# Optimization experiments

Measured on AMD Instinct MI355X. Metric: run time of the kernel, lower is better.

The kernel has to match this reference:

```python
import jax, jax.numpy as jnp
import numpy as np

B, S, H = 1, 1024, 2048          # batch, seq, hidden_size
I = 7168                          # intermediate_size
E = 8                             # num_local_experts
TOP_K = 2                         # num_experts_per_tok
R = int(I * H * 0.1 / (I + H))    # delta_low_rank = 159
SCALE = 0.02


def setup_inputs() -> dict:
    key = jax.random.key(0)
    ks = jax.random.split(key, 12)
    f = jnp.float32
    return {
        "x": jax.random.normal(ks[0], (B, S, H), dtype=f),
        "gate_w": jax.random.normal(ks[1], (E, H), dtype=f) * SCALE,
        "Wm1": jax.random.normal(ks[2], (I, H), dtype=f) * SCALE,  # Wmean1 (gate proj)
        "Wm2": jax.random.normal(ks[3], (H, I), dtype=f) * SCALE,  # Wmean2 (down proj)
        "Wm3": jax.random.normal(ks[4], (I, H), dtype=f) * SCALE,  # Wmean3 (up proj)
        "du1": jax.random.normal(ks[5], (E, I, R), dtype=f) * SCALE,
        "dv1": jax.random.normal(ks[6], (E, R, H), dtype=f) * SCALE,
        "du2": jax.random.normal(ks[7], (E, H, R), dtype=f) * SCALE,
        "dv2": jax.random.normal(ks[8], (E, R, I), dtype=f) * SCALE,
        "du3": jax.random.normal(ks[9], (E, I, R), dtype=f) * SCALE,
        "dv3": jax.random.normal(ks[10], (E, R, H), dtype=f) * SCALE,
    }


def reference(x, gate_w, Wm1, Wm2, Wm3, du1, dv1, du2, dv2, du3, dv3):
    b, s, h = x.shape
    hs = x.reshape(-1, h)                                  # [T, H]

    # --- router ---
    router_logits = hs @ gate_w.T                          # [T, E]
    probs = jax.nn.softmax(router_logits.astype(jnp.float32), axis=-1)
    top_w, top_i = jax.lax.top_k(probs, TOP_K)             # [T, K]
    top_w = top_w / jnp.sum(top_w, axis=-1, keepdims=True)
    # dense combine weights [T, E]: weight of expert e for token t (0 if not selected)
    comb = jnp.sum(jax.nn.one_hot(top_i, E, dtype=top_w.dtype) * top_w[..., None], axis=1)
    comb = comb.astype(hs.dtype)

    # --- shared mean weights (computed once per token) ---
    base_gate = hs @ Wm1.T                                 # [T, I]
    base_up = hs @ Wm3.T                                   # [T, I]

    # --- per-expert low-rank deltas ---
    t1 = jnp.einsum('th,erh->ter', hs, dv1)                # [T, E, R]
    gate = base_gate[:, None, :] + jnp.einsum('ter,eir->tei', t1, du1)  # [T, E, I]
    t3 = jnp.einsum('th,erh->ter', hs, dv3)
    up = base_up[:, None, :] + jnp.einsum('ter,eir->tei', t3, du3)      # [T, E, I]

    hmid = jax.nn.silu(gate) * up                          # [T, E, I]

    out = jnp.einsum('tei,hi->teh', hmid, Wm2)             # shared down proj
    t2 = jnp.einsum('tei,eri->ter', hmid, dv2)
    out = out + jnp.einsum('ter,ehr->teh', t2, du2)        # [T, E, H]

    final = jnp.einsum('te,teh->th', comb, out).reshape(b, s, h)
    return final, router_logits
```

## Files before the change

### kernel.cpp

```cpp
#include <hip/hip_runtime.h>

#define T_TOK 1024
#define H_DIM 2048
#define I_DIM 7168
#define E_NUM 8
#define R_RANK 159
#define RP 160
#define P_PAIRS 2048

typedef __attribute__((ext_vector_type(8))) short short8;
typedef __attribute__((ext_vector_type(4))) float f32x4;

__device__ __forceinline__ ushort f2b(float f) {
  uint u = __float_as_uint(f);
  uint r = (u + 0x7FFFu + ((u >> 16) & 1u)) >> 16;
  return (ushort)r;
}
__device__ __forceinline__ float b2f(ushort u) {
  return __uint_as_float(((uint)u) << 16);
}
__device__ __forceinline__ short8 pack8(float4 a, float4 b) {
  short8 o;
  o[0] = (short)f2b(a.x); o[1] = (short)f2b(a.y); o[2] = (short)f2b(a.z); o[3] = (short)f2b(a.w);
  o[4] = (short)f2b(b.x); o[5] = (short)f2b(b.y); o[6] = (short)f2b(b.z); o[7] = (short)f2b(b.w);
  return o;
}
__device__ __forceinline__ short8 zero8() {
  short8 z;
#pragma unroll
  for (int q = 0; q < 8; ++q) z[q] = 0;
  return z;
}

#define GLOAD(gptr, lptr) \
  __builtin_amdgcn_global_load_lds((const __attribute__((address_space(1))) void*)(gptr), \
                                   (__attribute__((address_space(3))) void*)(lptr), 16, 0, 0)

__global__ __launch_bounds__(256) void router_kernel(
    const float* __restrict__ x, const float* __restrict__ gw,
    float* __restrict__ logits, float* __restrict__ comb,
    int* __restrict__ sel_e, int* __restrict__ cnt) {
  int wave = threadIdx.x >> 6, lane = threadIdx.x & 63;
  int t = blockIdx.x * 4 + wave;
  const float* xr = x + (long)t * H_DIM;
  float acc[8] = {0.f,0.f,0.f,0.f,0.f,0.f,0.f,0.f};
  for (int h = lane * 4; h < H_DIM; h += 256) {
    const float4 xv = *(const float4*)&xr[h];
#pragma unroll
    for (int e = 0; e < 8; ++e) {
      const float4 gv = *(const float4*)&gw[e * H_DIM + h];
      acc[e] += xv.x * gv.x + xv.y * gv.y + xv.z * gv.z + xv.w * gv.w;
    }
  }
#pragma unroll
  for (int off = 32; off > 0; off >>= 1)
#pragma unroll
    for (int e = 0; e < 8; ++e) acc[e] += __shfl_down(acc[e], off);
  if (lane == 0) {
#pragma unroll
    for (int e = 0; e < 8; ++e) logits[(long)t * 8 + e] = acc[e];
    int i0 = 0;
    for (int e = 1; e < 8; ++e) if (acc[e] > acc[i0]) i0 = e;
    int i1 = (i0 == 0) ? 1 : 0;
    for (int e = 0; e < 8; ++e) if (e != i0 && acc[e] > acc[i1]) i1 = e;
    float ee = __expf(acc[i1] - acc[i0]);
    float w0 = 1.f / (1.f + ee), w1 = ee / (1.f + ee);
    for (int e = 0; e < 8; ++e) comb[t * 8 + e] = 0.f;
    comb[t * 8 + i0] = w0;
    comb[t * 8 + i1] = w1;
    sel_e[t * 2] = i0;
    sel_e[t * 2 + 1] = i1;
    atomicAdd(&cnt[i0], 1);
    atomicAdd(&cnt[i1], 1);
  }
}

__global__ void init_kernel(int* cnt, int* cursor) {
  int i = threadIdx.x;
  if (i < 8) { cnt[i] = 0; cursor[i] = 0; }
}

__global__ void scan_kernel(const int* cnt, int* seg) {
  if (threadIdx.x == 0) {
    int s = 0;
    for (int e = 0; e < 8; ++e) { seg[e] = s; s += cnt[e]; }
    seg[8] = s;
  }
}

__global__ void assign_kernel(const int* __restrict__ sel_e, const float* __restrict__ comb,
                              const int* __restrict__ seg, int* __restrict__ cursor,
                              int* __restrict__ tok, float* __restrict__ wrow,
                              int* __restrict__ row_of) {
  int t = blockIdx.x * blockDim.x + threadIdx.x;
  if (t >= T_TOK) return;
  for (int k = 0; k < 2; ++k) {
    int e = sel_e[t * 2 + k];
    int pos = atomicAdd(&cursor[e], 1);
    int row = seg[e] + pos;
    tok[row] = t;
    wrow[row] = comb[t * 8 + e];
    row_of[t * 2 + k] = row;
  }
}

__global__ void cast8_kernel(const float* __restrict__ src, ushort* __restrict__ dst, long n8) {
  long idx = (long)blockIdx.x * blockDim.x + threadIdx.x;
  long stride = (long)gridDim.x * blockDim.x;
  for (long i = idx; i < n8; i += stride) {
    const float4 a = *(const float4*)&src[i * 8];
    const float4 b = *(const float4*)&src[i * 8 + 4];
    *(short8*)&dst[i * 8] = pack8(a, b);
  }
}

__global__ void padcast8_kernel(const float* __restrict__ src, ushort* __restrict__ dst, long rows) {
  long n8 = rows * (RP / 8);
  long idx = (long)blockIdx.x * blockDim.x + threadIdx.x;
  long stride = (long)gridDim.x * blockDim.x;
  for (long i = idx; i < n8; i += stride) {
    long row = i / (RP / 8);
    int c0 = (int)(i % (RP / 8)) * 8;
    short8 o;
#pragma unroll
    for (int j = 0; j < 8; ++j) {
      int c = c0 + j;
      o[j] = (c < R_RANK) ? (short)f2b(src[row * R_RANK + c]) : (short)0;
    }
    *(short8*)&dst[row * RP + c0] = o;
  }
}

__global__ void hcomb_kernel(const ushort* __restrict__ hmid, const int* __restrict__ row_of,
                             ushort* __restrict__ hc) {
  long idx = (long)blockIdx.x * blockDim.x + threadIdx.x;
  long total = (long)T_TOK * I_DIM / 8;
  if (idx >= total) return;
  long i = idx * 8;
  int t = (int)(i / I_DIM);
  int col = (int)(i % I_DIM);
  int r0 = row_of[t * 2], r1 = row_of[t * 2 + 1];
  const short8 a = *(const short8*)&hmid[(long)r0 * I_DIM + col];
  const short8 b = *(const short8*)&hmid[(long)r1 * I_DIM + col];
  short8 o;
#pragma unroll
  for (int j = 0; j < 8; ++j)
    o[j] = (short)f2b(b2f((ushort)a[j]) + b2f((ushort)b[j]));
  *(short8*)&hc[i] = o;
}

__global__ void finalfix_kernel(float* __restrict__ out, const ushort* __restrict__ delta,
                                const int* __restrict__ row_of) {
  long idx = (long)blockIdx.x * blockDim.x + threadIdx.x;
  long total = (long)T_TOK * H_DIM / 4;
  if (idx >= total) return;
  long i = idx * 4;
  int t = (int)(i / H_DIM);
  int col = (int)(i % H_DIM);
  int r0 = row_of[t * 2], r1 = row_of[t * 2 + 1];
  float4 d = *(float4*)&out[i];
  d.x += b2f(delta[(long)r0 * H_DIM + col + 0]) + b2f(delta[(long)r1 * H_DIM + col + 0]);
  d.y += b2f(delta[(long)r0 * H_DIM + col + 1]) + b2f(delta[(long)r1 * H_DIM + col + 1]);
  d.z += b2f(delta[(long)r0 * H_DIM + col + 2]) + b2f(delta[(long)r1 * H_DIM + col + 2]);
  d.w += b2f(delta[(long)r0 * H_DIM + col + 3]) + b2f(delta[(long)r1 * H_DIM + col + 3]);
  *(float4*)&out[i] = d;
}

__global__ void finalfixA_kernel(float* __restrict__ out, const float* __restrict__ dp,
                                 const ushort* __restrict__ delta, const int* __restrict__ row_of) {
  long idx = (long)blockIdx.x * blockDim.x + threadIdx.x;
  long total = (long)T_TOK * H_DIM / 4;
  if (idx >= total) return;
  long i = idx * 4;
  int t = (int)(i / H_DIM);
  int col = (int)(i % H_DIM);
  int r0 = row_of[t * 2], r1 = row_of[t * 2 + 1];
  const long plane = (long)T_TOK * H_DIM;
  float4 s = *(const float4*)&dp[i];
#pragma unroll
  for (int k = 1; k < 4; ++k) {
    const float4 q = *(const float4*)&dp[k * plane + i];
    s.x += q.x; s.y += q.y; s.z += q.z; s.w += q.w;
  }
  s.x += b2f(delta[(long)r0 * H_DIM + col + 0]) + b2f(delta[(long)r1 * H_DIM + col + 0]);
  s.y += b2f(delta[(long)r0 * H_DIM + col + 1]) + b2f(delta[(long)r1 * H_DIM + col + 1]);
  s.z += b2f(delta[(long)r0 * H_DIM + col + 2]) + b2f(delta[(long)r1 * H_DIM + col + 2]);
  s.w += b2f(delta[(long)r0 * H_DIM + col + 3]) + b2f(delta[(long)r1 * H_DIM + col + 3]);
  *(float4*)&out[i] = s;
}

template <int KS>
__global__ void reduce_cast_kernel(const float* __restrict__ P, long plane,
                                   ushort* __restrict__ out, long n) {
  long i = (long)blockIdx.x * blockDim.x + threadIdx.x;
  if (i >= n) return;
  float s = 0.f;
#pragma unroll
  for (int k = 0; k < KS; ++k) s += P[(long)k * plane + i];
  out[i] = f2b(s);
}

__global__ void reduce2_kernel(const float* __restrict__ p1, const float* __restrict__ p3,
                               ushort* __restrict__ t1g, ushort* __restrict__ t3g, long n) {
  long i = (long)blockIdx.x * blockDim.x + threadIdx.x;
  if (i >= 2 * n) return;
  const float* P = (i < n) ? p1 : p3;
  ushort* o = (i < n) ? t1g : t3g;
  long ii = (i < n) ? i : i - n;
  float s = 0.f;
#pragma unroll
  for (int k = 0; k < 8; ++k) s += P[(long)k * n + ii];
  o[ii] = f2b(s);
}


__device__ __forceinline__ void kloop_bf16(
    const ushort* ar0, const ushort* ar1,
    const ushort* br0, const ushort* br1,
    int K, ushort* As, ushort* Bs,
    int tid, int lane, int wm, int wn, f32x4 acc[4][4]) {
  for (int k0 = 0; k0 < K; k0 += 32) {
    __syncthreads();
    GLOAD(ar0 + k0, &As[tid * 8]);
    GLOAD(ar1 + k0, &As[(256 + tid) * 8]);
    GLOAD(br0 + k0, &Bs[tid * 8]);
    GLOAD(br1 + k0, &Bs[(256 + tid) * 8]);
    __syncthreads();
    short8 av[4], bv[4];
#pragma unroll
    for (int mi = 0; mi < 4; ++mi)
      av[mi] = *(const short8*)&As[(wm + mi * 16 + (lane & 15)) * 32 + (lane >> 4) * 8];
#pragma unroll
    for (int ni = 0; ni < 4; ++ni)
      bv[ni] = *(const short8*)&Bs[(wn + ni * 16 + (lane & 15)) * 32 + (lane >> 4) * 8];
#pragma unroll
    for (int mi = 0; mi < 4; ++mi)
#pragma unroll
      for (int ni = 0; ni < 4; ++ni)
        acc[mi][ni] = __builtin_amdgcn_mfma_f32_16x16x32_bf16(av[mi], bv[ni], acc[mi][ni], 0, 0, 0);
  }
}

__device__ __forceinline__ void epi_bf16(
    f32x4 acc[4][4], ushort* smem, int tid, int lane, int wm, int wn,
    int row0, int col0, int M, int Nvalid, int Npad, ushort* Cb, int ldc) {
  const int er = (lane >> 4) * 4, ec = lane & 15;
  __syncthreads();
#pragma unroll
  for (int mi = 0; mi < 4; ++mi)
#pragma unroll
    for (int ni = 0; ni < 4; ++ni)
#pragma unroll
      for (int j = 0; j < 4; ++j) {
        int rr = wm + mi * 16 + er + j;
        int c = wn + ni * 16 + ec;
        smem[rr * 128 + (c ^ ((rr & 7) << 3))] =
            (col0 + c < Nvalid) ? f2b(acc[mi][ni][j]) : (ushort)0;
      }
  __syncthreads();
  const int rl = tid >> 1, clb = (tid & 1) * 64;
  const int r = row0 + rl;
  if (r < M) {
    const int k8 = (rl & 7) << 3;
#pragma unroll
    for (int jj = 0; jj < 8; ++jj) {
      int cg = col0 + clb + jj * 8;
      if (cg < Npad) {
        short8 v = *(const short8*)&smem[rl * 128 + ((clb + jj * 8) ^ k8)];
        *(short8*)&Cb[(long)r * ldc + cg] = v;
      }
    }
  }
}


__global__ __launch_bounds__(256) void k_base(
    const ushort* __restrict__ xb, const ushort* __restrict__ w1b, const ushort* __restrict__ w3b,
    ushort* __restrict__ bgate, ushort* __restrict__ bup) {
  __shared__ ushort smem[16384];
  ushort* As = smem;
  ushort* Bs = smem + 4096;
  const ushort* B = blockIdx.z ? w3b : w1b;
  ushort* C = blockIdx.z ? bup : bgate;
  const int tid = threadIdx.x;
  const int lane = tid & 63, wave = tid >> 6;
  const int wm = (wave >> 1) * 64, wn = (wave & 1) * 64;
  const int row0 = blockIdx.y * 128, col0 = blockIdx.x * 128;
  const int sub_r = tid >> 2, sub_c = (tid & 3) * 8;
  const ushort* ar0 = xb + (long)(row0 + sub_r) * H_DIM + sub_c;
  const ushort* ar1 = xb + (long)(row0 + 64 + sub_r) * H_DIM + sub_c;
  const ushort* br0 = B + (long)(col0 + sub_r) * H_DIM + sub_c;
  const ushort* br1 = B + (long)(col0 + 64 + sub_r) * H_DIM + sub_c;
  f32x4 acc[4][4] = {};
  kloop_bf16(ar0, ar1, br0, br1, H_DIM, As, Bs, tid, lane, wm, wn, acc);
  epi_bf16(acc, smem, tid, lane, wm, wn, row0, col0, T_TOK, I_DIM, I_DIM, C, I_DIM);
}

__global__ __launch_bounds__(256) void k_t13(
    const ushort* __restrict__ xb, const ushort* __restrict__ dv1b, const ushort* __restrict__ dv3b,
    const int* __restrict__ tok, const int* __restrict__ seg, const int* __restrict__ cnt,
    float* __restrict__ p1, float* __restrict__ p3) {
  __shared__ ushort smem[8192];
  ushort* As = smem;
  ushort* Bs = smem + 4096;
  const int z = blockIdx.z;
  const int which = z & 1;
  const int eks = z >> 1;
  const int e = eks >> 3, ks = eks & 7;
  const int m0 = seg[e], M = cnt[e];
  const int row0 = blockIdx.y * 128, col0 = blockIdx.x * 128;
  if (row0 >= M) return;
  const int kbase = ks * 256;
  const ushort* Bsrc = (which ? dv3b : dv1b) + (long)e * R_RANK * H_DIM;
  float* P = which ? p3 : p1;
  const int tid = threadIdx.x;
  const int lane = tid & 63, wave = tid >> 6;
  const int wm = (wave >> 1) * 64, wn = (wave & 1) * 64;
  const int sub_r = tid >> 2, sub_c = (tid & 3) * 8;
  int r0c = row0 + sub_r;      if (r0c > M - 1) r0c = M - 1;
  int r1c = row0 + 64 + sub_r; if (r1c > M - 1) r1c = M - 1;
  const ushort* ar0 = xb + (long)tok[m0 + r0c] * H_DIM + kbase + sub_c;
  const ushort* ar1 = xb + (long)tok[m0 + r1c] * H_DIM + kbase + sub_c;
  int q0 = col0 + sub_r;      if (q0 > R_RANK - 1) q0 = R_RANK - 1;
  int q1 = col0 + 64 + sub_r; if (q1 > R_RANK - 1) q1 = R_RANK - 1;
  const ushort* br0 = Bsrc + (long)q0 * H_DIM + kbase + sub_c;
  const ushort* br1 = Bsrc + (long)q1 * H_DIM + kbase + sub_c;
  f32x4 acc[4][4] = {};
  kloop_bf16(ar0, ar1, br0, br1, 256, As, Bs, tid, lane, wm, wn, acc);
  const int er = (lane >> 4) * 4, ec = lane & 15;
  const long plane = (long)P_PAIRS * RP;
#pragma unroll
  for (int mi = 0; mi < 4; ++mi)
#pragma unroll
    for (int ni = 0; ni < 4; ++ni)
#pragma unroll
      for (int j = 0; j < 4; ++j) {
        int r = row0 + wm + mi * 16 + er + j;
        int c = col0 + wn + ni * 16 + ec;
        if (r < M && c < RP)
          P[(long)ks * plane + (long)(m0 + r) * RP + c] = (c < R_RANK) ? acc[mi][ni][j] : 0.f;
      }
}

__global__ __launch_bounds__(256) void k_phase2(
    const ushort* __restrict__ hc, const ushort* __restrict__ w2b,
    const ushort* __restrict__ hmidg, const ushort* __restrict__ dv2b,
    const int* __restrict__ seg, const int* __restrict__ cnt,
    float* __restrict__ dp, float* __restrict__ p2) {
  __shared__ ushort smem[8192];
  ushort* As = smem;
  ushort* Bs = smem + 4096;
  const int tid = threadIdx.x;
  const int lane = tid & 63, wave = tid >> 6;
  const int wm = (wave >> 1) * 64, wn = (wave & 1) * 64;
  const int sub_r = tid >> 2, sub_c = (tid & 3) * 8;
  const int er = (lane >> 4) * 4, ec = lane & 15;

  if (blockIdx.z < 4) {
    const int ks = blockIdx.z;
    const int kbase = ks * (I_DIM / 4);
    const int row0 = blockIdx.y * 128, col0 = blockIdx.x * 128;
    const ushort* ar0 = hc + (long)(row0 + sub_r) * I_DIM + kbase + sub_c;
    const ushort* ar1 = hc + (long)(row0 + 64 + sub_r) * I_DIM + kbase + sub_c;
    const ushort* br0 = w2b + (long)(col0 + sub_r) * I_DIM + kbase + sub_c;
    const ushort* br1 = w2b + (long)(col0 + 64 + sub_r) * I_DIM + kbase + sub_c;
    f32x4 acc[4][4] = {};
    kloop_bf16(ar0, ar1, br0, br1, I_DIM / 4, As, Bs, tid, lane, wm, wn, acc);
    float* Pk = dp + (long)ks * T_TOK * H_DIM;
#pragma unroll
    for (int mi = 0; mi < 4; ++mi)
#pragma unroll
      for (int ni = 0; ni < 4; ++ni)
#pragma unroll
        for (int j = 0; j < 4; ++j) {
          int r = row0 + wm + mi * 16 + er + j;
          int c = col0 + wn + ni * 16 + ec;
          Pk[(long)r * H_DIM + c] = acc[mi][ni][j];
        }
  } else {
    const int f = (blockIdx.z - 4) * 128 + blockIdx.y * 16 + blockIdx.x;
    const int eks = f >> 4;
    const int e = eks >> 3, ks = eks & 7;
    const int rsub = f & 15;
    const int x2 = rsub & 1, y2 = rsub >> 1;
    const int m0 = seg[e], M = cnt[e];
    const int row0 = y2 * 128, col0 = x2 * 128;
    if (row0 >= M) return;
    const int kbase = ks * (I_DIM / 8);
    int r0c = row0 + sub_r;      if (r0c > M - 1) r0c = M - 1;
    int r1c = row0 + 64 + sub_r; if (r1c > M - 1) r1c = M - 1;
    const ushort* ar0 = hmidg + (long)(m0 + r0c) * I_DIM + kbase + sub_c;
    const ushort* ar1 = hmidg + (long)(m0 + r1c) * I_DIM + kbase + sub_c;
    int q0 = col0 + sub_r;      if (q0 > R_RANK - 1) q0 = R_RANK - 1;
    int q1 = col0 + 64 + sub_r; if (q1 > R_RANK - 1) q1 = R_RANK - 1;
    const ushort* br0 = dv2b + (long)e * R_RANK * I_DIM + (long)q0 * I_DIM + kbase + sub_c;
    const ushort* br1 = dv2b + (long)e * R_RANK * I_DIM + (long)q1 * I_DIM + kbase + sub_c;
    f32x4 acc[4][4] = {};
    kloop_bf16(ar0, ar1, br0, br1, I_DIM / 8, As, Bs, tid, lane, wm, wn, acc);
    const long plane = (long)P_PAIRS * RP;
#pragma unroll
    for (int mi = 0; mi < 4; ++mi)
#pragma unroll
      for (int ni = 0; ni < 4; ++ni)
#pragma unroll
        for (int j = 0; j < 4; ++j) {
          int r = row0 + wm + mi * 16 + er + j;
          int c = col0 + wn + ni * 16 + ec;
          if (r < M && c < RP)
            p2[(long)ks * plane + (long)(m0 + r) * RP + c] = (c < R_RANK) ? acc[mi][ni][j] : 0.f;
        }
  }
}

__global__ __launch_bounds__(256) void k_delta(
    const ushort* __restrict__ t2g, const ushort* __restrict__ du2b,
    const int* __restrict__ seg, const int* __restrict__ cnt,
    ushort* __restrict__ deltab) {
  __shared__ ushort smem[16384];
  ushort* As = smem;
  ushort* Bs = smem + 4096;
  const int e = blockIdx.z;
  const int m0 = seg[e], M = cnt[e];
  const int row0 = blockIdx.y * 128, col0 = blockIdx.x * 128;
  if (row0 >= M) return;
  const int tid = threadIdx.x;
  const int lane = tid & 63, wave = tid >> 6;
  const int wm = (wave >> 1) * 64, wn = (wave & 1) * 64;
  const int sub_r = tid >> 2, sub_c = (tid & 3) * 8;
  int r0c = row0 + sub_r;      if (r0c > M - 1) r0c = M - 1;
  int r1c = row0 + 64 + sub_r; if (r1c > M - 1) r1c = M - 1;
  const ushort* ar0 = t2g + (long)(m0 + r0c) * RP + sub_c;
  const ushort* ar1 = t2g + (long)(m0 + r1c) * RP + sub_c;
  const ushort* br0 = du2b + (long)e * H_DIM * RP + (long)(col0 + sub_r) * RP + sub_c;
  const ushort* br1 = du2b + (long)e * H_DIM * RP + (long)(col0 + 64 + sub_r) * RP + sub_c;
  f32x4 acc[4][4] = {};
  kloop_bf16(ar0, ar1, br0, br1, RP, As, Bs, tid, lane, wm, wn, acc);
  epi_bf16(acc, smem, tid, lane, wm, wn, row0, col0, M, H_DIM, H_DIM,
           deltab + (long)m0 * H_DIM, H_DIM);
}

__global__ __launch_bounds__(256) void gemm_hmid(
    const ushort* __restrict__ t1g, const ushort* __restrict__ t3g,
    const ushort* __restrict__ du1b, const ushort* __restrict__ du3b,
    const ushort* __restrict__ bgate, const ushort* __restrict__ bup,
    const int* __restrict__ tok, const float* __restrict__ wrow,
    const int* __restrict__ seg, const int* __restrict__ cnt,
    ushort* __restrict__ hmid) {
  __shared__ ushort smem[16384];
  ushort* As1 = smem;
  ushort* As3 = smem + 4096;
  ushort* Bs1 = smem + 8192;
  ushort* Bs3 = smem + 12288;
  int e = blockIdx.z;
  int m0 = seg[e], M = cnt[e];
  if ((int)(blockIdx.y * 128) >= M) return;
  const ushort* A1 = t1g + (long)m0 * RP;
  const ushort* A3 = t3g + (long)m0 * RP;
  const ushort* B1 = du1b + (long)e * I_DIM * RP;
  const ushort* B3 = du3b + (long)e * I_DIM * RP;
  tok += m0; wrow += m0;
  ushort* H = hmid + (long)m0 * I_DIM;

  const int tid = threadIdx.x;
  const int lane = tid & 63, wave = tid >> 6;
  const int wm = (wave >> 1) * 64, wn = (wave & 1) * 64;
  const int row0 = blockIdx.y * 128, col0 = blockIdx.x * 128;
  const int sub_r = tid >> 2;
  const int sub_c = (tid & 3) * 8;

  const ushort *a1r[2], *a3r[2], *b1r[2], *b3r[2];
#pragma unroll
  for (int p = 0; p < 2; ++p) {
    int r = row0 + p * 64 + sub_r; if (r > M - 1) r = M - 1;
    a1r[p] = A1 + (long)r * RP + sub_c;
    a3r[p] = A3 + (long)r * RP + sub_c;
    int q = col0 + p * 64 + sub_r; if (q > I_DIM - 1) q = I_DIM - 1;
    b1r[p] = B1 + (long)q * RP + sub_c;
    b3r[p] = B3 + (long)q * RP + sub_c;
  }

  f32x4 acc1[4][4] = {}, acc3[4][4] = {};

  for (int k0 = 0; k0 < RP; k0 += 32) {
    __syncthreads();
#pragma unroll
    for (int p = 0; p < 2; ++p) {
      GLOAD(a1r[p] + k0, &As1[(p * 256 + tid) * 8]);
      GLOAD(a3r[p] + k0, &As3[(p * 256 + tid) * 8]);
      GLOAD(b1r[p] + k0, &Bs1[(p * 256 + tid) * 8]);
      GLOAD(b3r[p] + k0, &Bs3[(p * 256 + tid) * 8]);
    }
    __syncthreads();

    short8 av1[4], av3[4], bv1[4], bv3[4];
#pragma unroll
    for (int mi = 0; mi < 4; ++mi) {
      av1[mi] = *(const short8*)&As1[(wm + mi * 16 + (lane & 15)) * 32 + (lane >> 4) * 8];
      av3[mi] = *(const short8*)&As3[(wm + mi * 16 + (lane & 15)) * 32 + (lane >> 4) * 8];
    }
#pragma unroll
    for (int ni = 0; ni < 4; ++ni) {
      bv1[ni] = *(const short8*)&Bs1[(wn + ni * 16 + (lane & 15)) * 32 + (lane >> 4) * 8];
      bv3[ni] = *(const short8*)&Bs3[(wn + ni * 16 + (lane & 15)) * 32 + (lane >> 4) * 8];
    }
#pragma unroll
    for (int mi = 0; mi < 4; ++mi)
#pragma unroll
      for (int ni = 0; ni < 4; ++ni) {
        acc1[mi][ni] = __builtin_amdgcn_mfma_f32_16x16x32_bf16(av1[mi], bv1[ni], acc1[mi][ni], 0, 0, 0);
        acc3[mi][ni] = __builtin_amdgcn_mfma_f32_16x16x32_bf16(av3[mi], bv3[ni], acc3[mi][ni], 0, 0, 0);
      }
  }

  const int er = (lane >> 4) * 4;
  const int ec = lane & 15;
  __syncthreads();
  ushort* Cs = smem;
#pragma unroll
  for (int mi = 0; mi < 4; ++mi)
#pragma unroll
    for (int ni = 0; ni < 4; ++ni)
#pragma unroll
      for (int j = 0; j < 4; ++j) {
        int rr = wm + mi * 16 + er + j;
        int c = wn + ni * 16 + ec;
        Cs[rr * 128 + (c ^ ((rr & 7) << 3))] = f2b(acc1[mi][ni][j]);
      }
  __syncthreads();
  const int rl = tid >> 1;
  const int clb = (tid & 1) * 64;
  const int r = row0 + rl;
  const bool rok = (r < M);
  const int t = rok ? tok[r] : 0;
  const float w = rok ? wrow[r] : 0.f;
  const int k8 = (rl & 7) << 3;
  uint svp[32];
#pragma unroll
  for (int jj = 0; jj < 8; ++jj) {
    short8 gb = zero8();
    if (rok) gb = *(const short8*)&bgate[(long)t * I_DIM + col0 + clb + jj * 8];
    short8 gv = *(const short8*)&Cs[rl * 128 + ((clb + jj * 8) ^ k8)];
#pragma unroll
    for (int q = 0; q < 8; q += 2) {
      float g0 = b2f((ushort)gv[q]) + b2f((ushort)gb[q]);
      float g1 = b2f((ushort)gv[q + 1]) + b2f((ushort)gb[q + 1]);
      float s0 = g0 / (1.f + __expf(-g0));
      float s1 = g1 / (1.f + __expf(-g1));
      svp[jj * 4 + q / 2] = (uint)f2b(s0) | ((uint)f2b(s1) << 16);
    }
  }
  __syncthreads();
#pragma unroll
  for (int mi = 0; mi < 4; ++mi)
#pragma unroll
    for (int ni = 0; ni < 4; ++ni)
#pragma unroll
      for (int j = 0; j < 4; ++j) {
        int rr = wm + mi * 16 + er + j;
        int c = wn + ni * 16 + ec;
        Cs[rr * 128 + (c ^ ((rr & 7) << 3))] = f2b(acc3[mi][ni][j]);
      }
  __syncthreads();
#pragma unroll
  for (int jj = 0; jj < 8; ++jj) {
    short8 ub = zero8();
    if (rok) ub = *(const short8*)&bup[(long)t * I_DIM + col0 + clb + jj * 8];
    short8 uv = *(const short8*)&Cs[rl * 128 + ((clb + jj * 8) ^ k8)];
    short8 o;
#pragma unroll
    for (int q = 0; q < 8; q += 2) {
      uint sp = svp[jj * 4 + q / 2];
      float u0 = b2f((ushort)uv[q]) + b2f((ushort)ub[q]);
      float u1 = b2f((ushort)uv[q + 1]) + b2f((ushort)ub[q + 1]);
      o[q]     = (short)f2b(w * b2f((ushort)(sp & 0xFFFFu)) * u0);
      o[q + 1] = (short)f2b(w * b2f((ushort)(sp >> 16)) * u1);
    }
    if (rok) *(short8*)&H[(long)r * I_DIM + col0 + clb + jj * 8] = o;
  }
}

template <int AF32, int BF32, int CBF16, int PEREXP, int AMAP>
__global__ __launch_bounds__(256) void gemm_f(
    const void* __restrict__ Ap, int lda,
    const void* __restrict__ Bp, int ldb, long Bstride,
    int M, int N, int K, int Npad,
    float* __restrict__ Cf, ushort* __restrict__ Cb, int ldc,
    const int* __restrict__ tok, const int* __restrict__ seg, const int* __restrict__ cnt) {
  __shared__ ushort smem[16384];
  ushort* As = smem;
  ushort* Bs = smem + 4096;
  const float* Af = (const float*)Ap;
  const ushort* Ab = (const ushort*)Ap;
  const float* Bf = (const float*)Bp;
  const ushort* Bb = (const ushort*)Bp;
  const int* amap = tok;
  if (PEREXP) {
    int e = blockIdx.z;
    int m0 = seg[e];
    M = cnt[e];
    if ((int)(blockIdx.y * 128) >= M) return;
    if (AMAP) {
      amap = tok + m0;
    } else {
      if (AF32) Af += (long)m0 * lda; else Ab += (long)m0 * lda;
    }
    if (BF32) Bf += (long)e * Bstride; else Bb += (long)e * Bstride;
    if (CBF16) Cb += (long)m0 * ldc; else Cf += (long)m0 * ldc;
  }
  const int tid = threadIdx.x;
  const int lane = tid & 63, wave = tid >> 6;
  const int wm = (wave >> 1) * 64, wn = (wave & 1) * 64;
  const int row0 = blockIdx.y * 128, col0 = blockIdx.x * 128;
  const int sub_r = tid >> 2;
  const int sub_c = (tid & 3) * 8;

  const float* afrow[2]; const ushort* abrow[2];
  const float* bfrow[2]; const ushort* bbrow[2];
#pragma unroll
  for (int p = 0; p < 2; ++p) {
    int r = row0 + p * 64 + sub_r; if (r > M - 1) r = M - 1;
    if (AMAP) r = amap[r];
    if (AF32) afrow[p] = Af + (long)r * lda + sub_c;
    else      abrow[p] = Ab + (long)r * lda + sub_c;
    int q = col0 + p * 64 + sub_r; if (q > N - 1) q = N - 1;
    if (BF32) bfrow[p] = Bf + (long)q * ldb + sub_c;
    else      bbrow[p] = Bb + (long)q * ldb + sub_c;
  }

  f32x4 acc[4][4] = {};

  for (int k0 = 0; k0 < K; k0 += 32) {
    float4 a0[2], a1[2], b0[2], b1[2];
    if (AF32) {
#pragma unroll
      for (int p = 0; p < 2; ++p) {
        a0[p] = *(const float4*)(afrow[p] + k0);
        a1[p] = *(const float4*)(afrow[p] + k0 + 4);
      }
    }
    if (BF32) {
#pragma unroll
      for (int p = 0; p < 2; ++p) {
        b0[p] = *(const float4*)(bfrow[p] + k0);
        b1[p] = *(const float4*)(bfrow[p] + k0 + 4);
      }
    }
    __syncthreads();
#pragma unroll
    for (int p = 0; p < 2; ++p) {
      if (AF32) {
        *(short8*)&As[(p * 256 + tid) * 8] = pack8(a0[p], a1[p]);
      } else {
        GLOAD(abrow[p] + k0, &As[(p * 256 + tid) * 8]);
      }
      if (BF32) {
        *(short8*)&Bs[(p * 256 + tid) * 8] = pack8(b0[p], b1[p]);
      } else {
        GLOAD(bbrow[p] + k0, &Bs[(p * 256 + tid) * 8]);
      }
    }
    __syncthreads();

    short8 av[4], bv[4];
#pragma unroll
    for (int mi = 0; mi < 4; ++mi)
      av[mi] = *(const short8*)&As[(wm + mi * 16 + (lane & 15)) * 32 + (lane >> 4) * 8];
#pragma unroll
    for (int ni = 0; ni < 4; ++ni)
      bv[ni] = *(const short8*)&Bs[(wn + ni * 16 + (lane & 15)) * 32 + (lane >> 4) * 8];
#pragma unroll
    for (int mi = 0; mi < 4; ++mi)
#pragma unroll
      for (int ni = 0; ni < 4; ++ni)
        acc[mi][ni] = __builtin_amdgcn_mfma_f32_16x16x32_bf16(av[mi], bv[ni], acc[mi][ni], 0, 0, 0);
  }

  const int er = (lane >> 4) * 4;
  const int ec = lane & 15;
  if (CBF16) {
    __syncthreads();
    ushort* Cs = smem;
#pragma unroll
    for (int mi = 0; mi < 4; ++mi)
#pragma unroll
      for (int ni = 0; ni < 4; ++ni)
#pragma unroll
        for (int j = 0; j < 4; ++j) {
          int rr = wm + mi * 16 + er + j;
          int c = wn + ni * 16 + ec;
          Cs[rr * 128 + (c ^ ((rr & 7) << 3))] =
              (col0 + c < N) ? f2b(acc[mi][ni][j]) : (ushort)0;
        }
    __syncthreads();
    const int rl = tid >> 1;
    const int clb = (tid & 1) * 64;
    const int r = row0 + rl;
    if (r < M) {
      const int k8 = (rl & 7) << 3;
#pragma unroll
      for (int jj = 0; jj < 8; ++jj) {
        int cg = col0 + clb + jj * 8;
        if (cg < Npad) {
          short8 v = *(const short8*)&Cs[rl * 128 + ((clb + jj * 8) ^ k8)];
          *(short8*)&Cb[(long)r * ldc + cg] = v;
        }
      }
    }
  } else {
#pragma unroll
    for (int mi = 0; mi < 4; ++mi)
#pragma unroll
      for (int ni = 0; ni < 4; ++ni)
#pragma unroll
        for (int j = 0; j < 4; ++j) {
          int r = row0 + wm + mi * 16 + er + j;
          int c = col0 + wn + ni * 16 + ec;
          if (r < M && c < Npad)
            Cf[(long)r * ldc + c] = (c < N) ? acc[mi][ni][j] : 0.f;
        }
  }
}

extern "C" void kernel_launch(void* const* d_in, const int* in_sizes, int n_in,
                              void* d_out, int out_size, void* d_ws, size_t ws_size,
                              hipStream_t stream) {
  const float* x   = (const float*)d_in[0];
  const float* gw  = (const float*)d_in[1];
  const float* Wm1 = (const float*)d_in[2];
  const float* Wm2 = (const float*)d_in[3];
  const float* Wm3 = (const float*)d_in[4];
  const float* du1 = (const float*)d_in[5];
  const float* dv1 = (const float*)d_in[6];
  const float* du2 = (const float*)d_in[7];
  const float* dv2 = (const float*)d_in[8];
  const float* du3 = (const float*)d_in[9];
  const float* dv3 = (const float*)d_in[10];

  float* out_final  = (float*)d_out;
  float* out_logits = out_final + (long)T_TOK * H_DIM;

  char* p = (char*)d_ws;
  auto alloc = [&](size_t bytes) {
    char* r = p;
    p += (bytes + 255) & ~(size_t)255;
    return r;
  };

  float* comb   = (float*)alloc((size_t)T_TOK * E_NUM * 4);
  float* wrow   = (float*)alloc((size_t)P_PAIRS * 4);
  int* cnt      = (int*)alloc(64);
  int* cursor   = (int*)alloc(64);
  int* seg      = (int*)alloc(64);
  int* sel_e    = (int*)alloc((size_t)T_TOK * 2 * 4);
  int* tok      = (int*)alloc((size_t)P_PAIRS * 4);
  int* row_of   = (int*)alloc((size_t)T_TOK * 2 * 4);
  ushort* bgate_b = (ushort*)alloc((size_t)T_TOK * I_DIM * 2);
  ushort* bup_b   = (ushort*)alloc((size_t)T_TOK * I_DIM * 2);
  ushort* hmidg   = (ushort*)alloc((size_t)P_PAIRS * I_DIM * 2);
  ushort* t1g     = (ushort*)alloc((size_t)P_PAIRS * RP * 2);
  ushort* t3g     = (ushort*)alloc((size_t)P_PAIRS * RP * 2);
  ushort* t2g     = (ushort*)alloc((size_t)P_PAIRS * RP * 2);
  ushort* du1b    = (ushort*)alloc((size_t)E_NUM * I_DIM * RP * 2);
  ushort* du3b    = (ushort*)alloc((size_t)E_NUM * I_DIM * RP * 2);
  ushort* du2b    = (ushort*)alloc((size_t)E_NUM * H_DIM * RP * 2);
  size_t needed_B = (size_t)(p - (char*)d_ws);
  ushort* xb   = (ushort*)alloc((size_t)T_TOK * H_DIM * 2);
  ushort* w1b  = (ushort*)alloc((size_t)I_DIM * H_DIM * 2);
  ushort* w3b  = (ushort*)alloc((size_t)I_DIM * H_DIM * 2);
  ushort* dv1b = (ushort*)alloc((size_t)E_NUM * R_RANK * H_DIM * 2);
  ushort* dv3b = (ushort*)alloc((size_t)E_NUM * R_RANK * H_DIM * 2);
  size_t needed_A = (size_t)(p - (char*)d_ws);
  ushort* w2b_d  = (ushort*)alloc((size_t)I_DIM * H_DIM * 2);
  ushort* dv2b_d = (ushort*)alloc((size_t)E_NUM * R_RANK * I_DIM * 2);
  size_t needed_A2 = (size_t)(p - (char*)d_ws);

  ushort* hc     = bgate_b;
  ushort* deltab = bup_b;

  if (ws_size < needed_B) return;
  const bool planA  = (ws_size >= needed_A);
  const bool planA2 = (ws_size >= needed_A2);

  dim3 blk(256);

  init_kernel<<<1, 64, 0, stream>>>(cnt, cursor);
  router_kernel<<<T_TOK / 4, 256, 0, stream>>>(x, gw, out_logits, comb, sel_e, cnt);
  scan_kernel<<<1, 64, 0, stream>>>(cnt, seg);
  assign_kernel<<<4, 256, 0, stream>>>(sel_e, comb, seg, cursor, tok, wrow, row_of);

  padcast8_kernel<<<4480, 256, 0, stream>>>(du1, du1b, (long)E_NUM * I_DIM);
  padcast8_kernel<<<4480, 256, 0, stream>>>(du3, du3b, (long)E_NUM * I_DIM);
  padcast8_kernel<<<1280, 256, 0, stream>>>(du2, du2b, (long)E_NUM * H_DIM);

  if (planA) {
    ushort* w2b  = planA2 ? w2b_d  : w1b;
    ushort* dv2b = planA2 ? dv2b_d : w3b;

    cast8_kernel<<<1024, 256, 0, stream>>>(x, xb, (long)T_TOK * H_DIM / 8);
    cast8_kernel<<<7168, 256, 0, stream>>>(Wm1, w1b, (long)I_DIM * H_DIM / 8);
    cast8_kernel<<<7168, 256, 0, stream>>>(Wm3, w3b, (long)I_DIM * H_DIM / 8);
    cast8_kernel<<<1272, 256, 0, stream>>>(dv1, dv1b, (long)E_NUM * R_RANK * H_DIM / 8);
    cast8_kernel<<<1272, 256, 0, stream>>>(dv3, dv3b, (long)E_NUM * R_RANK * H_DIM / 8);
    if (planA2) {
      cast8_kernel<<<7168, 256, 0, stream>>>(Wm2, w2b, (long)I_DIM * H_DIM / 8);
      cast8_kernel<<<4452, 256, 0, stream>>>(dv2, dv2b, (long)E_NUM * R_RANK * I_DIM / 8);
    }

    k_base<<<dim3(I_DIM / 128, T_TOK / 128, 2), blk, 0, stream>>>(xb, w1b, w3b, bgate_b, bup_b);

    float* p1 = (float*)hmidg;
    float* p3 = p1 + (long)8 * P_PAIRS * RP;
    k_t13<<<dim3(2, 8, 128), blk, 0, stream>>>(xb, dv1b, dv3b, tok, seg, cnt, p1, p3);
    reduce2_kernel<<<2560, 256, 0, stream>>>(p1, p3, t1g, t3g, (long)P_PAIRS * RP);

    if (!planA2) {
      cast8_kernel<<<7168, 256, 0, stream>>>(Wm2, w2b, (long)I_DIM * H_DIM / 8);
      cast8_kernel<<<4452, 256, 0, stream>>>(dv2, dv2b, (long)E_NUM * R_RANK * I_DIM / 8);
    }

    gemm_hmid<<<dim3(I_DIM / 128, 8, E_NUM), blk, 0, stream>>>(
        t1g, t3g, du1b, du3b, bgate_b, bup_b, tok, wrow, seg, cnt, hmidg);

    hcomb_kernel<<<(int)(((long)T_TOK * I_DIM / 8 + 255) / 256), 256, 0, stream>>>(hmidg, row_of, hc);

    float* dp = (float*)du1b;
    float* p2 = (float*)bup_b;
    k_phase2<<<dim3(H_DIM / 128, 8, 12), blk, 0, stream>>>(
        hc, w2b, hmidg, dv2b, seg, cnt, dp, p2);
    reduce_cast_kernel<8><<<1280, 256, 0, stream>>>(p2, (long)P_PAIRS * RP, t2g, (long)P_PAIRS * RP);

    k_delta<<<dim3(H_DIM / 128, 8, E_NUM), blk, 0, stream>>>(t2g, du2b, seg, cnt, deltab);

    finalfixA_kernel<<<2048, 256, 0, stream>>>(out_final, dp, deltab, row_of);
  } else {
    gemm_f<1, 1, 1, 0, 0><<<dim3(I_DIM / 128, T_TOK / 128, 1), blk, 0, stream>>>(
        x, H_DIM, Wm1, H_DIM, 0L, T_TOK, I_DIM, H_DIM, I_DIM,
        nullptr, bgate_b, I_DIM, nullptr, nullptr, nullptr);
    gemm_f<1, 1, 1, 0, 0><<<dim3(I_DIM / 128, T_TOK / 128, 1), blk, 0, stream>>>(
        x, H_DIM, Wm3, H_DIM, 0L, T_TOK, I_DIM, H_DIM, I_DIM,
        nullptr, bup_b, I_DIM, nullptr, nullptr, nullptr);
    gemm_f<1, 1, 1, 1, 1><<<dim3(2, 8, E_NUM), blk, 0, stream>>>(
        x, H_DIM, dv1, H_DIM, (long)R_RANK * H_DIM, 0, R_RANK, H_DIM, RP,
        nullptr, t1g, RP, tok, seg, cnt);
    gemm_f<1, 1, 1, 1, 1><<<dim3(2, 8, E_NUM), blk, 0, stream>>>(
        x, H_DIM, dv3, H_DIM, (long)R_RANK * H_DIM, 0, R_RANK, H_DIM, RP,
        nullptr, t3g, RP, tok, seg, cnt);
    gemm_hmid<<<dim3(I_DIM / 128, 8, E_NUM), blk, 0, stream>>>(
        t1g, t3g, du1b, du3b, bgate_b, bup_b, tok, wrow, seg, cnt, hmidg);
    hcomb_kernel<<<(int)(((long)T_TOK * I_DIM / 8 + 255) / 256), 256, 0, stream>>>(hmidg, row_of, hc);
    gemm_f<0, 1, 0, 0, 0><<<dim3(H_DIM / 128, T_TOK / 128, 1), blk, 0, stream>>>(
        hc, I_DIM, Wm2, I_DIM, 0L, T_TOK, H_DIM, I_DIM, H_DIM,
        out_final, nullptr, H_DIM, nullptr, nullptr, nullptr);
    gemm_f<0, 1, 1, 1, 0><<<dim3(2, 8, E_NUM), blk, 0, stream>>>(
        hmidg, I_DIM, dv2, I_DIM, (long)R_RANK * I_DIM, 0, R_RANK, I_DIM, RP,
        nullptr, t2g, RP, tok, seg, cnt);
    gemm_f<0, 0, 1, 1, 0><<<dim3(H_DIM / 128, 8, E_NUM), blk, 0, stream>>>(
        t2g, RP, du2b, RP, (long)H_DIM * RP, 0, H_DIM, RP, H_DIM,
        nullptr, deltab, H_DIM, tok, seg, cnt);
    finalfix_kernel<<<(int)(((long)T_TOK * H_DIM / 4 + 255) / 256), 256, 0, stream>>>(
        out_final, deltab, row_of);
  }
}
```

Measured before the change: 530.9 us.

## Swizzle LDS tile layout and double the K-step to 64 in bf16 GEMMs

Applies an XOR swizzle to the 8-element column groups of the 32-wide LDS tiles, on both the global-to-LDS load side and the MFMA fragment reads. This is meant to cut LDS bank conflicts. Most GEMM kernels (base, t13, down/t2) now use a new kloop64 that loads two 32-wide K slabs per barrier pair, halving the number of syncthreads per K. The cost is doubled shared memory per block (32KB), which may reduce occupancy. The small-K delta GEMM keeps the 32-step loop but with the swizzle.

```diff
diff --git a/kernel.cpp b/kernel.cpp
--- a/kernel.cpp
+++ b/kernel.cpp
@@ -31,6 +31,7 @@
   for (int q = 0; q < 8; ++q) z[q] = 0;
   return z;
 }
+__device__ __forceinline__ int swzofs(int row, int g) { return (g ^ ((row >> 1) & 3)) * 8; }
 
 #define GLOAD(gptr, lptr) \
   __builtin_amdgcn_global_load_lds((const __attribute__((address_space(1))) void*)(gptr), \
@@ -214,7 +215,7 @@
 }
 
 
-__device__ __forceinline__ void kloop_bf16(
+__device__ __forceinline__ void kloop32(
     const ushort* ar0, const ushort* ar1,
     const ushort* br0, const ushort* br1,
     int K, ushort* As, ushort* Bs,
@@ -228,16 +229,58 @@
     __syncthreads();
     short8 av[4], bv[4];
 #pragma unroll
-    for (int mi = 0; mi < 4; ++mi)
-      av[mi] = *(const short8*)&As[(wm + mi * 16 + (lane & 15)) * 32 + (lane >> 4) * 8];
-#pragma unroll
-    for (int ni = 0; ni < 4; ++ni)
-      bv[ni] = *(const short8*)&Bs[(wn + ni * 16 + (lane & 15)) * 32 + (lane >> 4) * 8];
+    for (int mi = 0; mi < 4; ++mi) {
+      int R = wm + mi * 16 + (lane & 15);
+      av[mi] = *(const short8*)&As[R * 32 + swzofs(R, lane >> 4)];
+    }
+#pragma unroll
+    for (int ni = 0; ni < 4; ++ni) {
+      int R = wn + ni * 16 + (lane & 15);
+      bv[ni] = *(const short8*)&Bs[R * 32 + swzofs(R, lane >> 4)];
+    }
 #pragma unroll
     for (int mi = 0; mi < 4; ++mi)
 #pragma unroll
       for (int ni = 0; ni < 4; ++ni)
         acc[mi][ni] = __builtin_amdgcn_mfma_f32_16x16x32_bf16(av[mi], bv[ni], acc[mi][ni], 0, 0, 0);
+  }
+}
+
+__device__ __forceinline__ void kloop64(
+    const ushort* ar0, const ushort* ar1,
+    const ushort* br0, const ushort* br1,
+    int K, ushort* As, ushort* Bs,
+    int tid, int lane, int wm, int wn, f32x4 acc[4][4]) {
+  for (int k0 = 0; k0 < K; k0 += 64) {
+    __syncthreads();
+    GLOAD(ar0 + k0,      &As[tid * 8]);
+    GLOAD(ar1 + k0,      &As[(256 + tid) * 8]);
+    GLOAD(ar0 + k0 + 32, &As[4096 + tid * 8]);
+    GLOAD(ar1 + k0 + 32, &As[4096 + (256 + tid) * 8]);
+    GLOAD(br0 + k0,      &Bs[tid * 8]);
+    GLOAD(br1 + k0,      &Bs[(256 + tid) * 8]);
+    GLOAD(br0 + k0 + 32, &Bs[4096 + tid * 8]);
+    GLOAD(br1 + k0 + 32, &Bs[4096 + (256 + tid) * 8]);
+    __syncthreads();
+#pragma unroll
+    for (int s = 0; s < 2; ++s) {
+      short8 av[4], bv[4];
+#pragma unroll
+      for (int mi = 0; mi < 4; ++mi) {
+        int R = wm + mi * 16 + (lane & 15);
+        av[mi] = *(const short8*)&As[s * 4096 + R * 32 + swzofs(R, lane >> 4)];
+      }
+#pragma unroll
+      for (int ni = 0; ni < 4; ++ni) {
+        int R = wn + ni * 16 + (lane & 15);
+        bv[ni] = *(const short8*)&Bs[s * 4096 + R * 32 + swzofs(R, lane >> 4)];
+      }
+#pragma unroll
+      for (int mi = 0; mi < 4; ++mi)
+#pragma unroll
+        for (int ni = 0; ni < 4; ++ni)
+          acc[mi][ni] = __builtin_amdgcn_mfma_f32_16x16x32_bf16(av[mi], bv[ni], acc[mi][ni], 0, 0, 0);
+    }
   }
 }
 
@@ -279,20 +322,20 @@
     ushort* __restrict__ bgate, ushort* __restrict__ bup) {
   __shared__ ushort smem[16384];
   ushort* As = smem;
-  ushort* Bs = smem + 4096;
+  ushort* Bs = smem + 8192;
   const ushort* B = blockIdx.z ? w3b : w1b;
   ushort* C = blockIdx.z ? bup : bgate;
   const int tid = threadIdx.x;
   const int lane = tid & 63, wave = tid >> 6;
   const int wm = (wave >> 1) * 64, wn = (wave & 1) * 64;
   const int row0 = blockIdx.y * 128, col0 = blockIdx.x * 128;
-  const int sub_r = tid >> 2, sub_c = (tid & 3) * 8;
+  const int sub_r = tid >> 2, sub_c = swzofs(sub_r, tid & 3);
   const ushort* ar0 = xb + (long)(row0 + sub_r) * H_DIM + sub_c;
   const ushort* ar1 = xb + (long)(row0 + 64 + sub_r) * H_DIM + sub_c;
   const ushort* br0 = B + (long)(col0 + sub_r) * H_DIM + sub_c;
   const ushort* br1 = B + (long)(col0 + 64 + sub_r) * H_DIM + sub_c;
   f32x4 acc[4][4] = {};
-  kloop_bf16(ar0, ar1, br0, br1, H_DIM, As, Bs, tid, lane, wm, wn, acc);
+  kloop64(ar0, ar1, br0, br1, H_DIM, As, Bs, tid, lane, wm, wn, acc);
   epi_bf16(acc, smem, tid, lane, wm, wn, row0, col0, T_TOK, I_DIM, I_DIM, C, I_DIM);
 }
 
@@ -300,9 +343,9 @@
     const ushort* __restrict__ xb, const ushort* __restrict__ dv1b, const ushort* __restrict__ dv3b,
     const int* __restrict__ tok, const int* __restrict__ seg, const int* __restrict__ cnt,
     float* __restrict__ p1, float* __restrict__ p3) {
-  __shared__ ushort smem[8192];
+  __shared__ ushort smem[16384];
   ushort* As = smem;
-  ushort* Bs = smem + 4096;
+  ushort* Bs = smem + 8192;
   const int z = blockIdx.z;
   const int which = z & 1;
   const int eks = z >> 1;
@@ -316,7 +359,7 @@
   const int tid = threadIdx.x;
   const int lane = tid & 63, wave = tid >> 6;
   const int wm = (wave >> 1) * 64, wn = (wave & 1) * 64;
-  const int sub_r = tid >> 2, sub_c = (tid & 3) * 8;
+  const int sub_r = tid >> 2, sub_c = swzofs(sub_r, tid & 3);
   int r0c = row0 + sub_r;      if (r0c > M - 1) r0c = M - 1;
   int r1c = row0 + 64 + sub_r; if (r1c > M - 1) r1c = M - 1;
   const ushort* ar0 = xb + (long)tok[m0 + r0c] * H_DIM + kbase + sub_c;
@@ -326,7 +369,7 @@
   const ushort* br0 = Bsrc + (long)q0 * H_DIM + kbase + sub_c;
   const ushort* br1 = Bsrc + (long)q1 * H_DIM + kbase + sub_c;
   f32x4 acc[4][4] = {};
-  kloop_bf16(ar0, ar1, br0, br1, 256, As, Bs, tid, lane, wm, wn, acc);
+  kloop64(ar0, ar1, br0, br1, 256, As, Bs, tid, lane, wm, wn, acc);
   const int er = (lane >> 4) * 4, ec = lane & 15;
   const long plane = (long)P_PAIRS * RP;
 #pragma unroll
@@ -347,13 +390,13 @@
     const ushort* __restrict__ hmidg, const ushort* __restrict__ dv2b,
     const int* __restrict__ seg, const int* __restrict__ cnt,
     float* __restrict__ dp, float* __restrict__ p2) {
-  __shared__ ushort smem[8192];
+  __shared__ ushort smem[16384];
   ushort* As = smem;
-  ushort* Bs = smem + 4096;
+  ushort* Bs = smem + 8192;
   const int tid = threadIdx.x;
   const int lane = tid & 63, wave = tid >> 6;
   const int wm = (wave >> 1) * 64, wn = (wave & 1) * 64;
-  const int sub_r = tid >> 2, sub_c = (tid & 3) * 8;
+  const int sub_r = tid >> 2, sub_c = swzofs(sub_r, tid & 3);
   const int er = (lane >> 4) * 4, ec = lane & 15;
 
   if (blockIdx.z < 4) {
@@ -365,7 +408,7 @@
     const ushort* br0 = w2b + (long)(col0 + sub_r) * I_DIM + kbase + sub_c;
     const ushort* br1 = w2b + (long)(col0 + 64 + sub_r) * I_DIM + kbase + sub_c;
     f32x4 acc[4][4] = {};
-    kloop_bf16(ar0, ar1, br0, br1, I_DIM / 4, As, Bs, tid, lane, wm, wn, acc);
+    kloop64(ar0, ar1, br0, br1, I_DIM / 4, As, Bs, tid, lane, wm, wn, acc);
     float* Pk = dp + (long)ks * T_TOK * H_DIM;
 #pragma unroll
     for (int mi = 0; mi < 4; ++mi)
@@ -396,7 +439,7 @@
     const ushort* br0 = dv2b + (long)e * R_RANK * I_DIM + (long)q0 * I_DIM + kbase + sub_c;
     const ushort* br1 = dv2b + (long)e * R_RANK * I_DIM + (long)q1 * I_DIM + kbase + sub_c;
     f32x4 acc[4][4] = {};
-    kloop_bf16(ar0, ar1, br0, br1, I_DIM / 8, As, Bs, tid, lane, wm, wn, acc);
+    kloop64(ar0, ar1, br0, br1, I_DIM / 8, As, Bs, tid, lane, wm, wn, acc);
     const long plane = (long)P_PAIRS * RP;
 #pragma unroll
     for (int mi = 0; mi < 4; ++mi)
@@ -426,7 +469,7 @@
   const int tid = threadIdx.x;
   const int lane = tid & 63, wave = tid >> 6;
   const int wm = (wave >> 1) * 64, wn = (wave & 1) * 64;
-  const int sub_r = tid >> 2, sub_c = (tid & 3) * 8;
+  const int sub_r = tid >> 2, sub_c = swzofs(sub_r, tid & 3);
   int r0c = row0 + sub_r;      if (r0c > M - 1) r0c = M - 1;
   int r1c = row0 + 64 + sub_r; if (r1c > M - 1) r1c = M - 1;
   const ushort* ar0 = t2g + (long)(m0 + r0c) * RP + sub_c;
@@ -434,7 +477,7 @@
   const ushort* br0 = du2b + (long)e * H_DIM * RP + (long)(col0 + sub_r) * RP + sub_c;
   const ushort* br1 = du2b + (long)e * H_DIM * RP + (long)(col0 + 64 + sub_r) * RP + sub_c;
   f32x4 acc[4][4] = {};
-  kloop_bf16(ar0, ar1, br0, br1, RP, As, Bs, tid, lane, wm, wn, acc);
+  kloop32(ar0, ar1, br0, br1, RP, As, Bs, tid, lane, wm, wn, acc);
   epi_bf16(acc, smem, tid, lane, wm, wn, row0, col0, M, H_DIM, H_DIM,
            deltab + (long)m0 * H_DIM, H_DIM);
 }
@@ -466,7 +509,7 @@
   const int wm = (wave >> 1) * 64, wn = (wave & 1) * 64;
   const int row0 = blockIdx.y * 128, col0 = blockIdx.x * 128;
   const int sub_r = tid >> 2;
-  const int sub_c = (tid & 3) * 8;
+  const int sub_c = swzofs(sub_r, tid & 3);
 
   const ushort *a1r[2], *a3r[2], *b1r[2], *b3r[2];
 #pragma unroll
@@ -495,13 +538,17 @@
     short8 av1[4], av3[4], bv1[4], bv3[4];
 #pragma unroll
     for (int mi = 0; mi < 4; ++mi) {
-      av1[mi] = *(const short8*)&As1[(wm + mi * 16 + (lane & 15)) * 32 + (lane >> 4) * 8];
-      av3[mi] = *(const short8*)&As3[(wm + mi * 16 + (lane & 15)) * 32 + (lane >> 4) * 8];
+      int R = wm + mi * 16 + (lane & 15);
+      int o = R * 32 + swzofs(R, lane >> 4);
+      av1[mi] = *(const short8*)&As1[o];
+      av3[mi] = *(const short8*)&As3[o];
     }
 #pragma unroll
     for (int ni = 0; ni < 4; ++ni) {
-      bv1[ni] = *(const short8*)&Bs1[(wn + ni * 16 + (lane & 15)) * 32 + (lane >> 4) * 8];
-      bv3[ni] = *(const short8*)&Bs3[(wn + ni * 16 + (lane & 15)) * 32 + (lane >> 4) * 8];
+      int R = wn + ni * 16 + (lane & 15);
+      int o = R * 32 + swzofs(R, lane >> 4);
+      bv1[ni] = *(const short8*)&Bs1[o];
+      bv3[ni] = *(const short8*)&Bs3[o];
     }
 #pragma unroll
     for (int mi = 0; mi < 4; ++mi)
```

After: 500.9 us. 5.7% less time.
